# Kernel optimization log

Hardware: AMD Instinct MI355X
Metric: run time of the kernel (lower is better)

## Reference

```python
import jax, jax.numpy as jnp
import numpy as np

HEADS = 8


def setup_inputs() -> dict:
    key = jax.random.key(0)
    ks = jax.random.split(key, 4)
    b, n, dim, inner = 8, 1024, 512, 512
    x = jax.random.normal(ks[0], (b, n, dim), jnp.float32)
    cp_mask = jax.random.randint(ks[1], (n, n), 0, 2, jnp.int32)  # binary core-periphery mask
    w_qkv = jax.random.normal(ks[2], (dim, 3 * inner), jnp.float32) * 0.02
    w_out = jax.random.normal(ks[3], (inner, dim), jnp.float32) * 0.02
    b_out = jnp.zeros((dim,), jnp.float32)
    return {"x": x, "cp_mask": cp_mask, "w_qkv": w_qkv, "w_out": w_out,
            "b_out": b_out, "patches_in_core_nodes": 16}


def reference(x, cp_mask, w_qkv, w_out, b_out, patches_in_core_nodes):
    b, n, dim = x.shape
    inner = w_qkv.shape[1] // 3
    dh = inner // HEADS
    scale = dh ** -0.5

    qkv = x @ w_qkv                                   # [b, n, 3*inner]
    q, k, v = jnp.split(qkv, 3, axis=-1)
    split_heads = lambda t: t.reshape(b, n, HEADS, dh).transpose(0, 2, 1, 3)
    q, k, v = map(split_heads, (q, k, v))             # [b, h, n, dh]

    mask = cp_mask.astype(x.dtype)                    # [n, n]
    dots_raw = jnp.einsum('bhnd,bhmd->bhnm', q, k)    # [b, h, n, n]

    # analysis pass: per-row mean |masked score|, summed over heads (detached in original)
    nnz = jnp.count_nonzero(cp_mask, axis=1).astype(x.dtype)       # [n]
    score = (jnp.abs(dots_raw * mask) * scale).sum(axis=1).sum(axis=-1) / nnz  # [b, n]
    score = jax.lax.stop_gradient(score)
    # original: list(np.argsort(score)) then list.reverse() -> batch order reversed
    idx = jnp.argsort(score, axis=-1)[::-1]           # [b, n]

    attn = jax.nn.softmax(dots_raw * scale * mask, axis=-1)
    out = jnp.einsum('bhnm,bhmd->bhnd', attn, v)      # [b, h, n, dh]
    out = out.transpose(0, 2, 1, 3).reshape(b, n, inner)

    # sequential row swap: out[j,i] <-> out[j,idx[j,i]] using the pristine clone
    out_clone = out
    bi = jnp.arange(b)
    for i in range(1, patches_in_core_nodes + 1):
        ti = idx[:, i]                                # [b]
        out = out.at[bi, i].set(out_clone[bi, ti])
        out = out.at[bi, ti].set(out_clone[:, i])
    return out @ w_out + b_out
```

## Files before the change

kernel.cpp:

```cpp
#include <hip/hip_runtime.h>
#include <hip/hip_bf16.h>

#define NN 1024
#define DH 64
#define DIM 512
#define INNER 512
#define QKV_N 1536
#define SCALE 0.125f
#define KPITCH 72

typedef short short8 __attribute__((ext_vector_type(8)));
typedef float floatx4 __attribute__((ext_vector_type(4)));

static __device__ __forceinline__ unsigned short f2bf(float x) {
  __hip_bfloat16 h = __float2bfloat16(x);
  unsigned short u;
  __builtin_memcpy(&u, &h, 2);
  return u;
}
static __device__ __forceinline__ void splitbf(float x, unsigned short& hi, unsigned short& lo) {
  __hip_bfloat16 h = __float2bfloat16(x);
  float hf = __bfloat162float(h);
  __hip_bfloat16 l = __float2bfloat16(x - hf);
  __builtin_memcpy(&hi, &h, 2);
  __builtin_memcpy(&lo, &l, 2);
}
static __device__ __forceinline__ void gll16(const unsigned short* g, unsigned short* l) {
  __builtin_amdgcn_global_load_lds(
      (const __attribute__((address_space(1))) unsigned int*)g,
      (__attribute__((address_space(3))) unsigned int*)l, 16, 0, 0);
}

__global__ __launch_bounds__(64) void nnz_kernel(const int* __restrict__ mask,
                                                 float* __restrict__ nnzf,
                                                 unsigned long long* __restrict__ Mbits) {
  int row = blockIdx.x;
  int lane = threadIdx.x;
  const int* mrow = mask + (size_t)row * NN;
  int tot = 0;
  for (int mt = 0; mt < 16; ++mt) {
    unsigned long long bits = __ballot(mrow[mt * 64 + lane] != 0);
    if (lane == 0) {
      Mbits[(size_t)row * 16 + mt] = bits;
      tot += __popcll(bits);
    }
  }
  if (lane == 0) nnzf[row] = (float)tot;
}

__global__ __launch_bounds__(256) void split_kernel(const float* __restrict__ in,
                                                    unsigned short* __restrict__ hi,
                                                    unsigned short* __restrict__ lo,
                                                    int n4) {
  int i = blockIdx.x * 256 + threadIdx.x;
  if (i >= n4) return;
  float4 v = ((const float4*)in)[i];
  ushort4 h, l;
  splitbf(v.x, h.x, l.x);
  splitbf(v.y, h.y, l.y);
  splitbf(v.z, h.z, l.z);
  splitbf(v.w, h.w, l.w);
  ((ushort4*)hi)[i] = h;
  ((ushort4*)lo)[i] = l;
}

__global__ __launch_bounds__(256) void tsplit_kernel(const float* __restrict__ in, int K, int N,
                                                     unsigned short* __restrict__ hiT,
                                                     unsigned short* __restrict__ loT) {
  __shared__ float tile[32][33];
  int n0 = blockIdx.x * 32, k0 = blockIdx.y * 32;
  int t = threadIdx.x;
  int tn = t & 31, tk = t >> 5;
#pragma unroll
  for (int i = 0; i < 32; i += 8)
    tile[tk + i][tn] = in[(size_t)(k0 + tk + i) * N + n0 + tn];
  __syncthreads();
#pragma unroll
  for (int i = 0; i < 32; i += 8) {
    int n = tk + i;
    float v = tile[tn][n];
    unsigned short h, l;
    splitbf(v, h, l);
    hiT[(size_t)(n0 + n) * K + k0 + tn] = h;
    loT[(size_t)(n0 + n) * K + k0 + tn] = l;
  }
}

__global__ __launch_bounds__(256) void qkv_mfma(const unsigned short* __restrict__ xhi,
                                                const unsigned short* __restrict__ xlo,
                                                const unsigned short* __restrict__ bhiT,
                                                const unsigned short* __restrict__ bloT,
                                                unsigned short* __restrict__ qhi,
                                                unsigned short* __restrict__ qlo,
                                                unsigned short* __restrict__ khi,
                                                unsigned short* __restrict__ klo,
                                                unsigned short* __restrict__ vb) {
  __shared__ __align__(16) unsigned short Ah[128 * 32], Al[128 * 32];
  __shared__ __align__(16) unsigned short Bh[128 * 32], Bl[128 * 32];
  int t = threadIdx.x;
  int lane = t & 63, w = t >> 6;
  int wr = w >> 1, wc = w & 1;
  int s = lane & 15, q4 = lane >> 4;
  int r0 = blockIdx.y * 128, c0 = blockIdx.x * 128;
  int kcol = (lane & 3) * 8;
  int rA = lane >> 2;

  floatx4 acc[4][4];
#pragma unroll
  for (int mi = 0; mi < 4; ++mi)
#pragma unroll
    for (int ni = 0; ni < 4; ++ni) { acc[mi][ni][0] = 0.f; acc[mi][ni][1] = 0.f; acc[mi][ni][2] = 0.f; acc[mi][ni][3] = 0.f; }

  for (int kt = 0; kt < DIM; kt += 32) {
    __syncthreads();
#pragma unroll
    for (int c = 0; c < 2; ++c) {
      int chunk = w * 2 + c;
      int row = chunk * 16 + rA;
      int lo_off = chunk * 512;
      gll16(&xhi[(size_t)(r0 + row) * DIM + kt + kcol], &Ah[lo_off]);
      gll16(&xlo[(size_t)(r0 + row) * DIM + kt + kcol], &Al[lo_off]);
      gll16(&bhiT[(size_t)(c0 + row) * DIM + kt + kcol], &Bh[lo_off]);
      gll16(&bloT[(size_t)(c0 + row) * DIM + kt + kcol], &Bl[lo_off]);
    }
    __syncthreads();
    short8 ah[4], al[4], bhf[4], blf[4];
#pragma unroll
    for (int mi = 0; mi < 4; ++mi) {
      ah[mi] = *(const short8*)&Ah[(wr * 64 + mi * 16 + s) * 32 + q4 * 8];
      al[mi] = *(const short8*)&Al[(wr * 64 + mi * 16 + s) * 32 + q4 * 8];
    }
#pragma unroll
    for (int ni = 0; ni < 4; ++ni) {
      bhf[ni] = *(const short8*)&Bh[(wc * 64 + ni * 16 + s) * 32 + q4 * 8];
      blf[ni] = *(const short8*)&Bl[(wc * 64 + ni * 16 + s) * 32 + q4 * 8];
    }
#pragma unroll
    for (int mi = 0; mi < 4; ++mi)
#pragma unroll
      for (int ni = 0; ni < 4; ++ni) {
        acc[mi][ni] = __builtin_amdgcn_mfma_f32_16x16x32_bf16(al[mi], bhf[ni], acc[mi][ni], 0, 0, 0);
        acc[mi][ni] = __builtin_amdgcn_mfma_f32_16x16x32_bf16(ah[mi], blf[ni], acc[mi][ni], 0, 0, 0);
        acc[mi][ni] = __builtin_amdgcn_mfma_f32_16x16x32_bf16(ah[mi], bhf[ni], acc[mi][ni], 0, 0, 0);
      }
  }

  int which = c0 >> 9;
#pragma unroll
  for (int mi = 0; mi < 4; ++mi)
#pragma unroll
    for (int ni = 0; ni < 4; ++ni) {
      int Cl = c0 + wc * 64 + ni * 16 + s;
      int cc = Cl & 511, h = cc >> 6, d = cc & 63;
#pragma unroll
      for (int i = 0; i < 4; ++i) {
        int R = r0 + wr * 64 + mi * 16 + q4 * 4 + i;
        int b = R >> 10, n = R & 1023;
        size_t o = (size_t)((((b << 3) + h) << 10) + n) * DH + d;
        float v = acc[mi][ni][i];
        if (which == 0) {
          unsigned short hh, ll;
          splitbf(SCALE * v, hh, ll);
          qhi[o] = hh; qlo[o] = ll;
        } else if (which == 1) {
          unsigned short hh, ll;
          splitbf(v, hh, ll);
          khi[o] = hh; klo[o] = ll;
        } else {
          vb[o] = f2bf(v);
        }
      }
    }
}

__global__ __launch_bounds__(256) void vtrans(const unsigned short* __restrict__ vb,
                                              unsigned short* __restrict__ vT) {
  int bh = blockIdx.y, nt = blockIdx.x;
  __shared__ __align__(16) unsigned short T[64][KPITCH];
  int t = threadIdx.x;
  {
    int n = t >> 2, d0 = (t & 3) * 16;
    const unsigned short* src = &vb[((size_t)bh * NN + nt * 64 + n) * DH + d0];
    *(short8*)&T[n][d0] = *(const short8*)&src[0];
    *(short8*)&T[n][d0 + 8] = *(const short8*)&src[8];
  }
  __syncthreads();
  {
    int d = t >> 2, n0 = (t & 3) * 16;
    short8 o0, o1;
#pragma unroll
    for (int j = 0; j < 8; ++j) {
      o0[j] = (short)T[n0 + j][d];
      o1[j] = (short)T[n0 + 8 + j][d];
    }
    unsigned short* dst = &vT[((size_t)bh * DH + d) * NN + nt * 64 + n0];
    *(short8*)&dst[0] = o0;
    *(short8*)&dst[8] = o1;
  }
}

__global__ __launch_bounds__(256, 4) void attn_kernel(const unsigned short* __restrict__ qhi,
                                                      const unsigned short* __restrict__ qlo,
                                                      const unsigned short* __restrict__ khi,
                                                      const unsigned short* __restrict__ klo,
                                                      const unsigned short* __restrict__ vT,
                                                      const unsigned long long* __restrict__ Mbits,
                                                      unsigned short* __restrict__ ohi,
                                                      unsigned short* __restrict__ olo,
                                                      float* __restrict__ sph) {
  int l = blockIdx.y * 16 + blockIdx.x;
  int k = l >> 3;
  int rb = k & 15;
  int bh = (l & 7) + 8 * (k >> 4);
  int b = bh >> 3, h = bh & 7;
  int row0 = rb * 64;
  int t = threadIdx.x;
  int lane = t & 63, w = t >> 6;
  int q4 = lane >> 4, s = lane & 15;
  int gr = 16 * w + s;

  __shared__ __align__(16) unsigned short Khs[64][KPITCH], Kls[64][KPITCH];
  __shared__ __align__(16) unsigned short Vts[64][KPITCH];
  __shared__ __align__(16) unsigned short Pss[64][KPITCH];
  __shared__ unsigned long long Mb[64];

  short8 aqh[2], aql[2];
  {
    size_t qb0 = ((size_t)bh * NN + row0 + gr) * DH;
#pragma unroll
    for (int ks = 0; ks < 2; ++ks) {
      aqh[ks] = *(const short8*)&qhi[qb0 + ks * 32 + q4 * 8];
      aql[ks] = *(const short8*)&qlo[qb0 + ks * 32 + q4 * 8];
    }
  }

  floatx4 Oacc[4];
  float Lacc[4], Sco[4];
#pragma unroll
  for (int j = 0; j < 4; ++j) { Oacc[j][0] = 0.f; Oacc[j][1] = 0.f; Oacc[j][2] = 0.f; Oacc[j][3] = 0.f; }
#pragma unroll
  for (int i = 0; i < 4; ++i) { Lacc[i] = 0.f; Sco[i] = 0.f; }

  for (int mt = 0; mt < 16; ++mt) {
    int m0 = mt * 64;
    __syncthreads();
#pragma unroll
    for (int p = 0; p < 2; ++p) {
      int idx = p * 256 + t;
      int n = idx >> 3, c8 = (idx & 7) * 8;
      size_t g = ((size_t)bh * NN + m0 + n) * DH + c8;
      *(short8*)&Khs[n][c8] = *(const short8*)&khi[g];
      *(short8*)&Kls[n][c8] = *(const short8*)&klo[g];
      *(short8*)&Vts[n][c8] = *(const short8*)&vT[((size_t)bh * DH + n) * NN + m0 + c8];
    }
    if (t < 64) Mb[t] = Mbits[(size_t)(row0 + t) * 16 + mt];
    __syncthreads();

    floatx4 Sf[4];
#pragma unroll
    for (int j = 0; j < 4; ++j) { Sf[j][0] = 0.f; Sf[j][1] = 0.f; Sf[j][2] = 0.f; Sf[j][3] = 0.f; }
#pragma unroll
    for (int ks = 0; ks < 2; ++ks) {
      int d0 = ks * 32 + q4 * 8;
#pragma unroll
      for (int j = 0; j < 4; ++j) {
        short8 kh8 = *(const short8*)&Khs[16 * j + s][d0];
        short8 kl8 = *(const short8*)&Kls[16 * j + s][d0];
        Sf[j] = __builtin_amdgcn_mfma_f32_16x16x32_bf16(aql[ks], kh8, Sf[j], 0, 0, 0);
        Sf[j] = __builtin_amdgcn_mfma_f32_16x16x32_bf16(aqh[ks], kl8, Sf[j], 0, 0, 0);
        Sf[j] = __builtin_amdgcn_mfma_f32_16x16x32_bf16(aqh[ks], kh8, Sf[j], 0, 0, 0);
      }
    }

    unsigned long long mb[4];
#pragma unroll
    for (int i = 0; i < 4; ++i) mb[i] = Mb[16 * w + 4 * q4 + i];
    unsigned short pw[4][4];
#pragma unroll
    for (int j = 0; j < 4; ++j) {
#pragma unroll
      for (int i = 0; i < 4; ++i) {
        float sv = Sf[j][i];
        float mf = ((mb[i] >> (16 * j + s)) & 1ULL) ? 1.0f : 0.0f;
        Sco[i] += fabsf(sv) * mf;
        float p = __expf(sv * mf);
        Lacc[i] += p;
        pw[i][j] = f2bf(p);
      }
    }

#pragma unroll
    for (int i = 0; i < 4; ++i)
#pragma unroll
      for (int j = 0; j < 4; ++j) Pss[16 * w + 4 * q4 + i][16 * j + s] = pw[i][j];

#pragma unroll
    for (int ks = 0; ks < 2; ++ks) {
      int mm0 = ks * 32 + q4 * 8;
      short8 ap = *(const short8*)&Pss[gr][mm0];
#pragma unroll
      for (int j = 0; j < 4; ++j) {
        short8 bv = *(const short8*)&Vts[16 * j + s][mm0];
        Oacc[j] = __builtin_amdgcn_mfma_f32_16x16x32_bf16(ap, bv, Oacc[j], 0, 0, 0);
      }
    }
  }

#pragma unroll
  for (int off = 1; off < 16; off <<= 1) {
#pragma unroll
    for (int i = 0; i < 4; ++i) {
      Lacc[i] += __shfl_xor(Lacc[i], off, 16);
      Sco[i] += __shfl_xor(Sco[i], off, 16);
    }
  }
#pragma unroll
  for (int i = 0; i < 4; ++i) {
    int r = row0 + 16 * w + 4 * q4 + i;
    float iv = 1.0f / Lacc[i];
#pragma unroll
    for (int j = 0; j < 4; ++j) {
      float o = Oacc[j][i] * iv;
      unsigned short hh, ll;
      splitbf(o, hh, ll);
      size_t oo = (size_t)((b << 10) + r) * INNER + (h << 6) + 16 * j + s;
      ohi[oo] = hh; olo[oo] = ll;
    }
    if (s == 0) sph[((size_t)bh << 10) + r] = Sco[i];
  }
}

__global__ __launch_bounds__(256) void score_select(const float* __restrict__ sph,
                                                    const float* __restrict__ nnzf,
                                                    const int* __restrict__ pic_ptr,
                                                    int* __restrict__ asc) {
  int bb = blockIdx.x;
  int t = threadIdx.x;
  int cnt = pic_ptr[0] + 1;
  float v[4];
#pragma unroll
  for (int i = 0; i < 4; ++i) {
    int r = t + 256 * i;
    float sv = 0.f;
#pragma unroll
    for (int h = 0; h < 8; ++h) sv += sph[(size_t)(((bb << 3) + h) << 10) + r];
    v[i] = sv / nnzf[r];
  }
  __shared__ float wv[4];
  __shared__ int wi[4];
  __shared__ int bsel;
  for (int sel = 0; sel < cnt; ++sel) {
    float bv = v[0];
    int bi = t;
#pragma unroll
    for (int i = 1; i < 4; ++i) {
      if (v[i] < bv) { bv = v[i]; bi = t + 256 * i; }
    }
#pragma unroll
    for (int off = 1; off < 64; off <<= 1) {
      float ov = __shfl_xor(bv, off, 64);
      int oi = __shfl_xor(bi, off, 64);
      if (ov < bv || (ov == bv && oi < bi)) { bv = ov; bi = oi; }
    }
    if ((t & 63) == 0) { wv[t >> 6] = bv; wi[t >> 6] = bi; }
    __syncthreads();
    if (t == 0) {
      float B = wv[0]; int I = wi[0];
#pragma unroll
      for (int q = 1; q < 4; ++q) {
        if (wv[q] < B || (wv[q] == B && wi[q] < I)) { B = wv[q]; I = wi[q]; }
      }
      bsel = I;
      asc[bb * 32 + sel] = I;
    }
    __syncthreads();
    int wloc = bsel - t;
    if (wloc >= 0 && (wloc & 255) == 0 && wloc < 1024) v[wloc >> 8] = 3.4e38f;
    __syncthreads();
  }
}

__global__ __launch_bounds__(256) void build_src(const int* __restrict__ asc,
                                                 const int* __restrict__ pic_ptr,
                                                 int* __restrict__ src) {
  int bi = blockIdx.x;
  int t = threadIdx.x;
  for (int r = t; r < 1024; r += 256) src[bi * 1024 + r] = r;
  __syncthreads();
  if (t == 0) {
    int pic = pic_ptr[0];
    const int* a = &asc[(7 - bi) * 32];
    for (int i = 1; i <= pic; ++i) {
      int ti = a[i];
      src[bi * 1024 + i] = ti;
      src[bi * 1024 + ti] = i;
    }
  }
}

__global__ __launch_bounds__(256) void out_mfma(const unsigned short* __restrict__ ahi,
                                                const unsigned short* __restrict__ alo,
                                                const unsigned short* __restrict__ bhiT,
                                                const unsigned short* __restrict__ bloT,
                                                const float* __restrict__ bias,
                                                const int* __restrict__ src,
                                                float* __restrict__ C) {
  __shared__ __align__(16) unsigned short Ah[128 * 32], Al[128 * 32];
  __shared__ __align__(16) unsigned short Bh[128 * 32], Bl[128 * 32];
  int t = threadIdx.x;
  int lane = t & 63, w = t >> 6;
  int wr = w >> 1, wc = w & 1;
  int s = lane & 15, q4 = lane >> 4;
  int r0 = blockIdx.y * 128, c0 = blockIdx.x * 128;
  int bb = r0 >> 10;
  int kcol = (lane & 3) * 8;
  int rA = lane >> 2;

  int grow[2];
#pragma unroll
  for (int c = 0; c < 2; ++c) {
    int row = (w * 2 + c) * 16 + rA;
    grow[c] = (bb << 10) + src[r0 + row];
  }

  floatx4 acc[4][4];
#pragma unroll
  for (int mi = 0; mi < 4; ++mi)
#pragma unroll
    for (int ni = 0; ni < 4; ++ni) { acc[mi][ni][0] = 0.f; acc[mi][ni][1] = 0.f; acc[mi][ni][2] = 0.f; acc[mi][ni][3] = 0.f; }

  for (int kt = 0; kt < INNER; kt += 32) {
    __syncthreads();
#pragma unroll
    for (int c = 0; c < 2; ++c) {
      int chunk = w * 2 + c;
      int row = chunk * 16 + rA;
      int lo_off = chunk * 512;
      gll16(&ahi[(size_t)grow[c] * INNER + kt + kcol], &Ah[lo_off]);
      gll16(&alo[(size_t)grow[c] * INNER + kt + kcol], &Al[lo_off]);
      gll16(&bhiT[(size_t)(c0 + row) * INNER + kt + kcol], &Bh[lo_off]);
      gll16(&bloT[(size_t)(c0 + row) * INNER + kt + kcol], &Bl[lo_off]);
    }
    __syncthreads();
    short8 ah[4], al[4], bhf[4], blf[4];
#pragma unroll
    for (int mi = 0; mi < 4; ++mi) {
      ah[mi] = *(const short8*)&Ah[(wr * 64 + mi * 16 + s) * 32 + q4 * 8];
      al[mi] = *(const short8*)&Al[(wr * 64 + mi * 16 + s) * 32 + q4 * 8];
    }
#pragma unroll
    for (int ni = 0; ni < 4; ++ni) {
      bhf[ni] = *(const short8*)&Bh[(wc * 64 + ni * 16 + s) * 32 + q4 * 8];
      blf[ni] = *(const short8*)&Bl[(wc * 64 + ni * 16 + s) * 32 + q4 * 8];
    }
#pragma unroll
    for (int mi = 0; mi < 4; ++mi)
#pragma unroll
      for (int ni = 0; ni < 4; ++ni) {
        acc[mi][ni] = __builtin_amdgcn_mfma_f32_16x16x32_bf16(al[mi], bhf[ni], acc[mi][ni], 0, 0, 0);
        acc[mi][ni] = __builtin_amdgcn_mfma_f32_16x16x32_bf16(ah[mi], blf[ni], acc[mi][ni], 0, 0, 0);
        acc[mi][ni] = __builtin_amdgcn_mfma_f32_16x16x32_bf16(ah[mi], bhf[ni], acc[mi][ni], 0, 0, 0);
      }
  }

#pragma unroll
  for (int ni = 0; ni < 4; ++ni) {
    int Cl = c0 + wc * 64 + ni * 16 + s;
    float bv = bias[Cl];
#pragma unroll
    for (int mi = 0; mi < 4; ++mi)
#pragma unroll
      for (int i = 0; i < 4; ++i) {
        int R = r0 + wr * 64 + mi * 16 + q4 * 4 + i;
        C[(size_t)R * DIM + Cl] = acc[mi][ni][i] + bv;
      }
  }
}

extern "C" void kernel_launch(void* const* d_in, const int* in_sizes, int n_in,
                              void* d_out, int out_size, void* d_ws, size_t ws_size,
                              hipStream_t stream) {
  const float* x      = (const float*)d_in[0];
  const int*   cpmask = (const int*)d_in[1];
  const float* w_qkv  = (const float*)d_in[2];
  const float* w_out  = (const float*)d_in[3];
  const float* b_out  = (const float*)d_in[4];
  const int*   pic    = (const int*)d_in[5];
  float* out = (float*)d_out;

  unsigned short* xhi   = (unsigned short*)d_ws;
  unsigned short* xlo   = xhi + 4194304;
  unsigned short* wqhiT = xlo + 4194304;
  unsigned short* wqloT = wqhiT + 786432;
  unsigned short* wohiT = wqloT + 786432;
  unsigned short* woloT = wohiT + 262144;
  unsigned short* qhi   = woloT + 262144;
  unsigned short* qlo   = qhi + 4194304;
  unsigned short* khi   = qlo + 4194304;
  unsigned short* klo   = khi + 4194304;
  unsigned short* vbp   = klo + 4194304;
  float* sph  = (float*)(vbp + 4194304);
  float* sc   = sph + 65536;
  float* nnzf = sc + 8192;
  int*   asc  = (int*)(nnzf + 1024);
  int*   src  = asc + 512;
  unsigned long long* Mbits = (unsigned long long*)(src + 8192);
  unsigned short* vTp = (unsigned short*)(Mbits + 16384);

  unsigned short* ohi = xhi;
  unsigned short* olo = xlo;

  hipLaunchKernelGGL(nnz_kernel,    dim3(1024),    dim3(64),  0, stream, cpmask, nnzf, Mbits);
  hipLaunchKernelGGL(split_kernel,  dim3(4096),    dim3(256), 0, stream, x, xhi, xlo, 1048576);
  hipLaunchKernelGGL(tsplit_kernel, dim3(48, 16),  dim3(256), 0, stream, w_qkv, DIM, QKV_N, wqhiT, wqloT);
  hipLaunchKernelGGL(tsplit_kernel, dim3(16, 16),  dim3(256), 0, stream, w_out, INNER, DIM, wohiT, woloT);
  hipLaunchKernelGGL(qkv_mfma,      dim3(12, 64),  dim3(256), 0, stream, xhi, xlo, wqhiT, wqloT,
                     qhi, qlo, khi, klo, vbp);
  hipLaunchKernelGGL(vtrans,        dim3(16, 64),  dim3(256), 0, stream, vbp, vTp);
  hipLaunchKernelGGL(attn_kernel,   dim3(16, 64),  dim3(256), 0, stream, qhi, qlo, khi, klo, vTp,
                     Mbits, ohi, olo, sph);
  hipLaunchKernelGGL(score_select,  dim3(8),       dim3(256), 0, stream, sph, nnzf, pic, asc);
  hipLaunchKernelGGL(build_src,     dim3(8),       dim3(256), 0, stream, asc, pic, src);
  hipLaunchKernelGGL(out_mfma,      dim3(4, 64),   dim3(256), 0, stream, ohi, olo, wohiT, woloT,
                     b_out, src, out);
}
```

Baseline: 258.6 us.

## Restage GEMMs with swizzled 64-wide K tiles, fuse V transpose, vectorize stores

The QKV and output GEMMs now stage 64-wide K tiles with XOR-swizzled LDS layouts, one operand plane per wave, and a 1D grid ordered by row tile. The V projection uses a single bf16 pass instead of three split passes and writes V transposed straight from an LDS staging tile, which removes the separate vtrans kernel. The attention kernel loads K, K-lo and V^T through async global-to-LDS copies into swizzled tiles, reads a mask-bits array transposed for coalescing, and writes its output through LDS as vectorized short8 stores. Together these target LDS bank conflicts, scattered 2-byte global stores and launch overhead, at the cost of a much larger QKV shared-memory footprint (about 66 KB) and lower occupancy.

```diff
diff --git a/kernel.cpp b/kernel.cpp
--- a/kernel.cpp
+++ b/kernel.cpp
@@ -7,7 +7,7 @@
 #define INNER 512
 #define QKV_N 1536
 #define SCALE 0.125f
-#define KPITCH 72
+#define PPITCH 72
 
 typedef short short8 __attribute__((ext_vector_type(8)));
 typedef float floatx4 __attribute__((ext_vector_type(4)));
@@ -41,7 +41,7 @@
   for (int mt = 0; mt < 16; ++mt) {
     unsigned long long bits = __ballot(mrow[mt * 64 + lane] != 0);
     if (lane == 0) {
-      Mbits[(size_t)row * 16 + mt] = bits;
+      Mbits[(size_t)mt * NN + row] = bits;
       tot += __popcll(bits);
     }
   }
@@ -94,16 +94,38 @@
                                                 unsigned short* __restrict__ qlo,
                                                 unsigned short* __restrict__ khi,
                                                 unsigned short* __restrict__ klo,
-                                                unsigned short* __restrict__ vb) {
-  __shared__ __align__(16) unsigned short Ah[128 * 32], Al[128 * 32];
-  __shared__ __align__(16) unsigned short Bh[128 * 32], Bl[128 * 32];
+                                                unsigned short* __restrict__ vT) {
+  __shared__ __align__(16) unsigned char smemQ[67584];
+  unsigned short* planeS = (unsigned short*)smemQ;
+  float* ct = (float*)smemQ;
+
+  int l = blockIdx.x;
+  int by = l & 63, bx = l >> 6;
+  int r0 = by * 128, c0 = bx * 128;
+  int which = c0 >> 9;
+  bool split3 = (which != 2);
   int t = threadIdx.x;
   int lane = t & 63, w = t >> 6;
   int wr = w >> 1, wc = w & 1;
   int s = lane & 15, q4 = lane >> 4;
-  int r0 = blockIdx.y * 128, c0 = blockIdx.x * 128;
-  int kcol = (lane & 3) * 8;
-  int rA = lane >> 2;
+  int sx7 = s & 7;
+  int r8 = lane >> 3, j7 = lane & 7;
+  int colsw = ((j7 ^ r8) << 3);
+
+  const unsigned short* gsrc;
+  int tb;
+  if (w == 0) { gsrc = xhi; tb = r0; }
+  else if (w == 1) { gsrc = xlo; tb = r0; }
+  else if (w == 2) { gsrc = bhiT; tb = c0; }
+  else { gsrc = bloT; tb = c0; }
+  unsigned short* lp = planeS + w * 8192;
+  const unsigned short* gp = gsrc + (size_t)(tb + r8) * DIM + colsw;
+  bool doStage = split3 || (w == 0) || (w == 2);
+
+  const unsigned short* Ah = planeS;
+  const unsigned short* Al = planeS + 8192;
+  const unsigned short* Bh = planeS + 16384;
+  const unsigned short* Bl = planeS + 24576;
 
   floatx4 acc[4][4];
 #pragma unroll
@@ -111,91 +133,106 @@
 #pragma unroll
     for (int ni = 0; ni < 4; ++ni) { acc[mi][ni][0] = 0.f; acc[mi][ni][1] = 0.f; acc[mi][ni][2] = 0.f; acc[mi][ni][3] = 0.f; }
 
-  for (int kt = 0; kt < DIM; kt += 32) {
-    __syncthreads();
-#pragma unroll
-    for (int c = 0; c < 2; ++c) {
-      int chunk = w * 2 + c;
-      int row = chunk * 16 + rA;
-      int lo_off = chunk * 512;
-      gll16(&xhi[(size_t)(r0 + row) * DIM + kt + kcol], &Ah[lo_off]);
-      gll16(&xlo[(size_t)(r0 + row) * DIM + kt + kcol], &Al[lo_off]);
-      gll16(&bhiT[(size_t)(c0 + row) * DIM + kt + kcol], &Bh[lo_off]);
-      gll16(&bloT[(size_t)(c0 + row) * DIM + kt + kcol], &Bl[lo_off]);
-    }
-    __syncthreads();
-    short8 ah[4], al[4], bhf[4], blf[4];
-#pragma unroll
-    for (int mi = 0; mi < 4; ++mi) {
-      ah[mi] = *(const short8*)&Ah[(wr * 64 + mi * 16 + s) * 32 + q4 * 8];
-      al[mi] = *(const short8*)&Al[(wr * 64 + mi * 16 + s) * 32 + q4 * 8];
-    }
-#pragma unroll
-    for (int ni = 0; ni < 4; ++ni) {
-      bhf[ni] = *(const short8*)&Bh[(wc * 64 + ni * 16 + s) * 32 + q4 * 8];
-      blf[ni] = *(const short8*)&Bl[(wc * 64 + ni * 16 + s) * 32 + q4 * 8];
-    }
+  for (int kt = 0; kt < DIM; kt += 64) {
+    __syncthreads();
+    if (doStage) {
+#pragma unroll
+      for (int ii = 0; ii < 16; ++ii)
+        gll16(gp + (size_t)ii * 8 * DIM + kt, lp + ii * 512);
+    }
+    __syncthreads();
+#pragma unroll
+    for (int ks2 = 0; ks2 < 2; ++ks2) {
+      int pc = ((ks2 * 4 + q4) ^ sx7) << 3;
+      short8 ah[4], al[4], bhf[4], blf[4];
+#pragma unroll
+      for (int mi = 0; mi < 4; ++mi) {
+        int ra = (wr * 64 + mi * 16 + s) * 64 + pc;
+        ah[mi] = *(const short8*)&Ah[ra];
+        if (split3) al[mi] = *(const short8*)&Al[ra];
+      }
+#pragma unroll
+      for (int ni = 0; ni < 4; ++ni) {
+        int rb = (wc * 64 + ni * 16 + s) * 64 + pc;
+        bhf[ni] = *(const short8*)&Bh[rb];
+        if (split3) blf[ni] = *(const short8*)&Bl[rb];
+      }
+#pragma unroll
+      for (int mi = 0; mi < 4; ++mi)
+#pragma unroll
+        for (int ni = 0; ni < 4; ++ni) {
+          if (split3) {
+            acc[mi][ni] = __builtin_amdgcn_mfma_f32_16x16x32_bf16(al[mi], bhf[ni], acc[mi][ni], 0, 0, 0);
+            acc[mi][ni] = __builtin_amdgcn_mfma_f32_16x16x32_bf16(ah[mi], blf[ni], acc[mi][ni], 0, 0, 0);
+          }
+          acc[mi][ni] = __builtin_amdgcn_mfma_f32_16x16x32_bf16(ah[mi], bhf[ni], acc[mi][ni], 0, 0, 0);
+        }
+    }
+  }
+
+  __syncthreads();
+  if (which != 2) {
+    float sc = (which == 0) ? SCALE : 1.0f;
 #pragma unroll
     for (int mi = 0; mi < 4; ++mi)
 #pragma unroll
-      for (int ni = 0; ni < 4; ++ni) {
-        acc[mi][ni] = __builtin_amdgcn_mfma_f32_16x16x32_bf16(al[mi], bhf[ni], acc[mi][ni], 0, 0, 0);
-        acc[mi][ni] = __builtin_amdgcn_mfma_f32_16x16x32_bf16(ah[mi], blf[ni], acc[mi][ni], 0, 0, 0);
-        acc[mi][ni] = __builtin_amdgcn_mfma_f32_16x16x32_bf16(ah[mi], bhf[ni], acc[mi][ni], 0, 0, 0);
-      }
-  }
-
-  int which = c0 >> 9;
-#pragma unroll
-  for (int mi = 0; mi < 4; ++mi)
-#pragma unroll
-    for (int ni = 0; ni < 4; ++ni) {
-      int Cl = c0 + wc * 64 + ni * 16 + s;
-      int cc = Cl & 511, h = cc >> 6, d = cc & 63;
-#pragma unroll
-      for (int i = 0; i < 4; ++i) {
-        int R = r0 + wr * 64 + mi * 16 + q4 * 4 + i;
-        int b = R >> 10, n = R & 1023;
-        size_t o = (size_t)((((b << 3) + h) << 10) + n) * DH + d;
-        float v = acc[mi][ni][i];
-        if (which == 0) {
-          unsigned short hh, ll;
-          splitbf(SCALE * v, hh, ll);
-          qhi[o] = hh; qlo[o] = ll;
-        } else if (which == 1) {
-          unsigned short hh, ll;
-          splitbf(v, hh, ll);
-          khi[o] = hh; klo[o] = ll;
-        } else {
-          vb[o] = f2bf(v);
-        }
-      }
-    }
-}
-
-__global__ __launch_bounds__(256) void vtrans(const unsigned short* __restrict__ vb,
-                                              unsigned short* __restrict__ vT) {
-  int bh = blockIdx.y, nt = blockIdx.x;
-  __shared__ __align__(16) unsigned short T[64][KPITCH];
-  int t = threadIdx.x;
-  {
-    int n = t >> 2, d0 = (t & 3) * 16;
-    const unsigned short* src = &vb[((size_t)bh * NN + nt * 64 + n) * DH + d0];
-    *(short8*)&T[n][d0] = *(const short8*)&src[0];
-    *(short8*)&T[n][d0 + 8] = *(const short8*)&src[8];
+      for (int ni = 0; ni < 4; ++ni)
+#pragma unroll
+        for (int i = 0; i < 4; ++i)
+          ct[(wr * 64 + mi * 16 + q4 * 4 + i) * 132 + (wc * 64 + ni * 16 + s)] = acc[mi][ni][i] * sc;
+  } else {
+#pragma unroll
+    for (int mi = 0; mi < 4; ++mi)
+#pragma unroll
+      for (int ni = 0; ni < 4; ++ni)
+#pragma unroll
+        for (int i = 0; i < 4; ++i)
+          ct[(wc * 64 + ni * 16 + s) * 132 + (wr * 64 + mi * 16 + q4 * 4 + i)] = acc[mi][ni][i];
   }
   __syncthreads();
-  {
-    int d = t >> 2, n0 = (t & 3) * 16;
-    short8 o0, o1;
-#pragma unroll
-    for (int j = 0; j < 8; ++j) {
-      o0[j] = (short)T[n0 + j][d];
-      o1[j] = (short)T[n0 + 8 + j][d];
-    }
-    unsigned short* dst = &vT[((size_t)bh * DH + d) * NN + nt * 64 + n0];
-    *(short8*)&dst[0] = o0;
-    *(short8*)&dst[8] = o1;
+  if (which != 2) {
+    int tr = t >> 1, ch = t & 1;
+    int R = r0 + tr, b = R >> 10, n = R & 1023;
+    int h0 = ((c0 & 511) >> 6) + ch;
+    unsigned short* dhi = (which == 0) ? qhi : khi;
+    unsigned short* dlo = (which == 0) ? qlo : klo;
+    size_t go = ((size_t)(((b << 3) + h0) << 10) + n) * DH;
+#pragma unroll
+    for (int u = 0; u < 4; ++u) {
+      const float* src = &ct[tr * 132 + ch * 64 + u * 16];
+      short8 h8a, h8b, l8a, l8b;
+#pragma unroll
+      for (int e = 0; e < 8; ++e) {
+        unsigned short hh, ll;
+        splitbf(src[e], hh, ll);
+        h8a[e] = (short)hh; l8a[e] = (short)ll;
+        splitbf(src[8 + e], hh, ll);
+        h8b[e] = (short)hh; l8b[e] = (short)ll;
+      }
+      *(short8*)&dhi[go + u * 16] = h8a;
+      *(short8*)&dhi[go + u * 16 + 8] = h8b;
+      *(short8*)&dlo[go + u * 16] = l8a;
+      *(short8*)&dlo[go + u * 16 + 8] = l8b;
+    }
+  } else {
+    int cr = t >> 1, th = t & 1;
+    int b = r0 >> 10;
+    int hglob = ((c0 & 511) >> 6) + (cr >> 6);
+    int d = cr & 63;
+    int n0 = (r0 & 1023) + th * 64;
+    size_t go = ((size_t)(((b << 3) + hglob) * DH) + d) * NN + n0;
+#pragma unroll
+    for (int u = 0; u < 4; ++u) {
+      const float* src = &ct[cr * 132 + th * 64 + u * 16];
+      short8 o0, o1;
+#pragma unroll
+      for (int e = 0; e < 8; ++e) {
+        o0[e] = (short)f2bf(src[e]);
+        o1[e] = (short)f2bf(src[8 + e]);
+      }
+      *(short8*)&vT[go + u * 16] = o0;
+      *(short8*)&vT[go + u * 16 + 8] = o1;
+    }
   }
 }
 
@@ -204,7 +241,7 @@
                                                       const unsigned short* __restrict__ khi,
                                                       const unsigned short* __restrict__ klo,
                                                       const unsigned short* __restrict__ vT,
-                                                      const unsigned long long* __restrict__ Mbits,
+                                                      const unsigned long long* __restrict__ MbT,
                                                       unsigned short* __restrict__ ohi,
                                                       unsigned short* __restrict__ olo,
                                                       float* __restrict__ sph) {
@@ -217,12 +254,22 @@
   int t = threadIdx.x;
   int lane = t & 63, w = t >> 6;
   int q4 = lane >> 4, s = lane & 15;
+  int sx7 = s & 7;
   int gr = 16 * w + s;
-
-  __shared__ __align__(16) unsigned short Khs[64][KPITCH], Kls[64][KPITCH];
-  __shared__ __align__(16) unsigned short Vts[64][KPITCH];
-  __shared__ __align__(16) unsigned short Pss[64][KPITCH];
+  int r8 = lane >> 3, j7 = lane & 7;
+  int colsw = ((j7 ^ r8) << 3);
+
+  __shared__ __align__(16) unsigned short stageS[3 * 4096];
+  __shared__ __align__(16) unsigned short Ps[64 * PPITCH];
   __shared__ unsigned long long Mb[64];
+  unsigned short* Khs = stageS;
+  unsigned short* Kls = stageS + 4096;
+  unsigned short* Vts = stageS + 8192;
+  float* Ofl = (float*)stageS;
+
+  const unsigned short* khp = khi + ((size_t)bh * NN + 16 * w + r8) * DH + colsw;
+  const unsigned short* klp = klo + ((size_t)bh * NN + 16 * w + r8) * DH + colsw;
+  const unsigned short* vtp = vT + ((size_t)bh * DH + 16 * w + r8) * NN + colsw;
 
   short8 aqh[2], aql[2];
   {
@@ -242,18 +289,15 @@
   for (int i = 0; i < 4; ++i) { Lacc[i] = 0.f; Sco[i] = 0.f; }
 
   for (int mt = 0; mt < 16; ++mt) {
-    int m0 = mt * 64;
-    __syncthreads();
-#pragma unroll
-    for (int p = 0; p < 2; ++p) {
-      int idx = p * 256 + t;
-      int n = idx >> 3, c8 = (idx & 7) * 8;
-      size_t g = ((size_t)bh * NN + m0 + n) * DH + c8;
-      *(short8*)&Khs[n][c8] = *(const short8*)&khi[g];
-      *(short8*)&Kls[n][c8] = *(const short8*)&klo[g];
-      *(short8*)&Vts[n][c8] = *(const short8*)&vT[((size_t)bh * DH + n) * NN + m0 + c8];
-    }
-    if (t < 64) Mb[t] = Mbits[(size_t)(row0 + t) * 16 + mt];
+    __syncthreads();
+#pragma unroll
+    for (int ii = 0; ii < 2; ++ii) {
+      int lofs = (16 * w + 8 * ii) * 64;
+      gll16(khp + (size_t)mt * 64 * DH + (size_t)ii * 8 * DH, Khs + lofs);
+      gll16(klp + (size_t)mt * 64 * DH + (size_t)ii * 8 * DH, Kls + lofs);
+      gll16(vtp + (size_t)mt * 64 + (size_t)ii * 8 * NN, Vts + lofs);
+    }
+    if (t < 64) Mb[t] = MbT[(size_t)mt * NN + row0 + t];
     __syncthreads();
 
     floatx4 Sf[4];
@@ -261,11 +305,12 @@
     for (int j = 0; j < 4; ++j) { Sf[j][0] = 0.f; Sf[j][1] = 0.f; Sf[j][2] = 0.f; Sf[j][3] = 0.f; }
 #pragma unroll
     for (int ks = 0; ks < 2; ++ks) {
-      int d0 = ks * 32 + q4 * 8;
+      int pc = ((ks * 4 + q4) ^ sx7) << 3;
 #pragma unroll
       for (int j = 0; j < 4; ++j) {
-        short8 kh8 = *(const short8*)&Khs[16 * j + s][d0];
-        short8 kl8 = *(const short8*)&Kls[16 * j + s][d0];
+        int rk = (16 * j + s) * 64 + pc;
+        short8 kh8 = *(const short8*)&Khs[rk];
+        short8 kl8 = *(const short8*)&Kls[rk];
         Sf[j] = __builtin_amdgcn_mfma_f32_16x16x32_bf16(aql[ks], kh8, Sf[j], 0, 0, 0);
         Sf[j] = __builtin_amdgcn_mfma_f32_16x16x32_bf16(aqh[ks], kl8, Sf[j], 0, 0, 0);
         Sf[j] = __builtin_amdgcn_mfma_f32_16x16x32_bf16(aqh[ks], kh8, Sf[j], 0, 0, 0);
@@ -292,15 +337,16 @@
 #pragma unroll
     for (int i = 0; i < 4; ++i)
 #pragma unroll
-      for (int j = 0; j < 4; ++j) Pss[16 * w + 4 * q4 + i][16 * j + s] = pw[i][j];
+      for (int j = 0; j < 4; ++j) Ps[(16 * w + 4 * q4 + i) * PPITCH + 16 * j + s] = pw[i][j];
 
 #pragma unroll
     for (int ks = 0; ks < 2; ++ks) {
       int mm0 = ks * 32 + q4 * 8;
-      short8 ap = *(const short8*)&Pss[gr][mm0];
+      short8 ap = *(const short8*)&Ps[gr * PPITCH + mm0];
+      int pc = ((ks * 4 + q4) ^ sx7) << 3;
 #pragma unroll
       for (int j = 0; j < 4; ++j) {
-        short8 bv = *(const short8*)&Vts[16 * j + s][mm0];
+        short8 bv = *(const short8*)&Vts[(16 * j + s) * 64 + pc];
         Oacc[j] = __builtin_amdgcn_mfma_f32_16x16x32_bf16(ap, bv, Oacc[j], 0, 0, 0);
       }
     }
@@ -314,19 +360,39 @@
       Sco[i] += __shfl_xor(Sco[i], off, 16);
     }
   }
+  if (s == 0) {
+#pragma unroll
+    for (int i = 0; i < 4; ++i)
+      sph[((size_t)bh << 10) + row0 + 16 * w + 4 * q4 + i] = Sco[i];
+  }
+
+  __syncthreads();
 #pragma unroll
   for (int i = 0; i < 4; ++i) {
-    int r = row0 + 16 * w + 4 * q4 + i;
     float iv = 1.0f / Lacc[i];
 #pragma unroll
-    for (int j = 0; j < 4; ++j) {
-      float o = Oacc[j][i] * iv;
+    for (int j = 0; j < 4; ++j)
+      Ofl[(16 * w + 4 * q4 + i) * 68 + 16 * j + s] = Oacc[j][i] * iv;
+  }
+  __syncthreads();
+  {
+    int tr = t >> 2, dq = t & 3;
+    int r = row0 + tr;
+    size_t go = ((size_t)((b << 10) + r)) * INNER + (h << 6) + dq * 16;
+    const float* src = &Ofl[tr * 68 + dq * 16];
+    short8 h8a, h8b, l8a, l8b;
+#pragma unroll
+    for (int e = 0; e < 8; ++e) {
       unsigned short hh, ll;
-      splitbf(o, hh, ll);
-      size_t oo = (size_t)((b << 10) + r) * INNER + (h << 6) + 16 * j + s;
-      ohi[oo] = hh; olo[oo] = ll;
-    }
-    if (s == 0) sph[((size_t)bh << 10) + r] = Sco[i];
+      splitbf(src[e], hh, ll);
+      h8a[e] = (short)hh; l8a[e] = (short)ll;
+      splitbf(src[8 + e], hh, ll);
+      h8b[e] = (short)hh; l8b[e] = (short)ll;
+    }
+    *(short8*)&ohi[go] = h8a;
+    *(short8*)&ohi[go + 8] = h8b;
+    *(short8*)&olo[go] = l8a;
+    *(short8*)&olo[go + 8] = l8b;
   }
 }
 
@@ -405,23 +471,31 @@
                                                 const float* __restrict__ bias,
                                                 const int* __restrict__ src,
                                                 float* __restrict__ C) {
-  __shared__ __align__(16) unsigned short Ah[128 * 32], Al[128 * 32];
-  __shared__ __align__(16) unsigned short Bh[128 * 32], Bl[128 * 32];
+  __shared__ __align__(16) unsigned short planeS[4 * 8192];
+  int l = blockIdx.x;
+  int by = l & 63, bx = l >> 6;
+  int r0 = by * 128, c0 = bx * 128;
   int t = threadIdx.x;
   int lane = t & 63, w = t >> 6;
   int wr = w >> 1, wc = w & 1;
   int s = lane & 15, q4 = lane >> 4;
-  int r0 = blockIdx.y * 128, c0 = blockIdx.x * 128;
-  int bb = r0 >> 10;
-  int kcol = (lane & 3) * 8;
-  int rA = lane >> 2;
-
-  int grow[2];
-#pragma unroll
-  for (int c = 0; c < 2; ++c) {
-    int row = (w * 2 + c) * 16 + rA;
-    grow[c] = (bb << 10) + src[r0 + row];
-  }
+  int sx7 = s & 7;
+  int r8 = lane >> 3, j7 = lane & 7;
+  int colsw = ((j7 ^ r8) << 3);
+  int bb1024 = (r0 >> 10) << 10;
+
+  int srcrow[16];
+  if (w < 2) {
+#pragma unroll
+    for (int ii = 0; ii < 16; ++ii) srcrow[ii] = src[r0 + ii * 8 + r8];
+  }
+  const unsigned short* gsrc = (w == 0) ? ahi : (w == 1) ? alo : (w == 2) ? bhiT : bloT;
+  unsigned short* lp = planeS + w * 8192;
+
+  const unsigned short* Ah = planeS;
+  const unsigned short* Al = planeS + 8192;
+  const unsigned short* Bh = planeS + 16384;
+  const unsigned short* Bl = planeS + 24576;
 
   floatx4 acc[4][4];
 #pragma unroll
@@ -429,38 +503,43 @@
 #pragma unroll
     for (int ni = 0; ni < 4; ++ni) { acc[mi][ni][0] = 0.f; acc[mi][ni][1] = 0.f; acc[mi][ni][2] = 0.f; acc[mi][ni][3] = 0.f; }
 
-  for (int kt = 0; kt < INNER; kt += 32) {
-    __syncthreads();
-#pragma unroll
-    for (int c = 0; c < 2; ++c) {
-      int chunk = w * 2 + c;
-      int row = chunk * 16 + rA;
-      int lo_off = chunk * 512;
-      gll16(&ahi[(size_t)grow[c] * INNER + kt + kcol], &Ah[lo_off]);
-      gll16(&alo[(size_t)grow[c] * INNER + kt + kcol], &Al[lo_off]);
-      gll16(&bhiT[(size_t)(c0 + row) * INNER + kt + kcol], &Bh[lo_off]);
-      gll16(&bloT[(size_t)(c0 + row) * INNER + kt + kcol], &Bl[lo_off]);
-    }
-    __syncthreads();
-    short8 ah[4], al[4], bhf[4], blf[4];
-#pragma unroll
-    for (int mi = 0; mi < 4; ++mi) {
-      ah[mi] = *(const short8*)&Ah[(wr * 64 + mi * 16 + s) * 32 + q4 * 8];
-      al[mi] = *(const short8*)&Al[(wr * 64 + mi * 16 + s) * 32 + q4 * 8];
-    }
-#pragma unroll
-    for (int ni = 0; ni < 4; ++ni) {
-      bhf[ni] = *(const short8*)&Bh[(wc * 64 + ni * 16 + s) * 32 + q4 * 8];
-      blf[ni] = *(const short8*)&Bl[(wc * 64 + ni * 16 + s) * 32 + q4 * 8];
-    }
-#pragma unroll
-    for (int mi = 0; mi < 4; ++mi)
+  for (int kt = 0; kt < INNER; kt += 64) {
+    __syncthreads();
+    if (w < 2) {
+#pragma unroll
+      for (int ii = 0; ii < 16; ++ii)
+        gll16(gsrc + (size_t)(bb1024 + srcrow[ii]) * INNER + kt + colsw, lp + ii * 512);
+    } else {
+#pragma unroll
+      for (int ii = 0; ii < 16; ++ii)
+        gll16(gsrc + (size_t)(c0 + ii * 8 + r8) * INNER + kt + colsw, lp + ii * 512);
+    }
+    __syncthreads();
+#pragma unroll
+    for (int ks2 = 0; ks2 < 2; ++ks2) {
+      int pc = ((ks2 * 4 + q4) ^ sx7) << 3;
+      short8 ah[4], al[4], bhf[4], blf[4];
+#pragma unroll
+      for (int mi = 0; mi < 4; ++mi) {
+        int ra = (wr * 64 + mi * 16 + s) * 64 + pc;
+        ah[mi] = *(const short8*)&Ah[ra];
+        al[mi] = *(const short8*)&Al[ra];
+      }
 #pragma unroll
       for (int ni = 0; ni < 4; ++ni) {
-        acc[mi][ni] = __builtin_amdgcn_mfma_f32_16x16x32_bf16(al[mi], bhf[ni], acc[mi][ni], 0, 0, 0);
-        acc[mi][ni] = __builtin_amdgcn_mfma_f32_16x16x32_bf16(ah[mi], blf[ni], acc[mi][ni], 0, 0, 0);
-        acc[mi][ni] = __builtin_amdgcn_mfma_f32_16x16x32_bf16(ah[mi], bhf[ni], acc[mi][ni], 0, 0, 0);
-      }
+        int rb = (wc * 64 + ni * 16 + s) * 64 + pc;
+        bhf[ni] = *(const short8*)&Bh[rb];
+        blf[ni] = *(const short8*)&Bl[rb];
+      }
+#pragma unroll
+      for (int mi = 0; mi < 4; ++mi)
+#pragma unroll
+        for (int ni = 0; ni < 4; ++ni) {
+          acc[mi][ni] = __builtin_amdgcn_mfma_f32_16x16x32_bf16(al[mi], bhf[ni], acc[mi][ni], 0, 0, 0);
+          acc[mi][ni] = __builtin_amdgcn_mfma_f32_16x16x32_bf16(ah[mi], blf[ni], acc[mi][ni], 0, 0, 0);
+          acc[mi][ni] = __builtin_amdgcn_mfma_f32_16x16x32_bf16(ah[mi], bhf[ni], acc[mi][ni], 0, 0, 0);
+        }
+    }
   }
 
 #pragma unroll
@@ -514,13 +593,12 @@
   hipLaunchKernelGGL(split_kernel,  dim3(4096),    dim3(256), 0, stream, x, xhi, xlo, 1048576);
   hipLaunchKernelGGL(tsplit_kernel, dim3(48, 16),  dim3(256), 0, stream, w_qkv, DIM, QKV_N, wqhiT, wqloT);
   hipLaunchKernelGGL(tsplit_kernel, dim3(16, 16),  dim3(256), 0, stream, w_out, INNER, DIM, wohiT, woloT);
-  hipLaunchKernelGGL(qkv_mfma,      dim3(12, 64),  dim3(256), 0, stream, xhi, xlo, wqhiT, wqloT,
-                     qhi, qlo, khi, klo, vbp);
-  hipLaunchKernelGGL(vtrans,        dim3(16, 64),  dim3(256), 0, stream, vbp, vTp);
+  hipLaunchKernelGGL(qkv_mfma,      dim3(768),     dim3(256), 0, stream, xhi, xlo, wqhiT, wqloT,
+                     qhi, qlo, khi, klo, vTp);
   hipLaunchKernelGGL(attn_kernel,   dim3(16, 64),  dim3(256), 0, stream, qhi, qlo, khi, klo, vTp,
                      Mbits, ohi, olo, sph);
   hipLaunchKernelGGL(score_select,  dim3(8),       dim3(256), 0, stream, sph, nnzf, pic, asc);
   hipLaunchKernelGGL(build_src,     dim3(8),       dim3(256), 0, stream, asc, pic, src);
-  hipLaunchKernelGGL(out_mfma,      dim3(4, 64),   dim3(256), 0, stream, ohi, olo, wohiT, woloT,
+  hipLaunchKernelGGL(out_mfma,      dim3(256),     dim3(256), 0, stream, ohi, olo, wohiT, woloT,
                      b_out, src, out);
 }
```

Result: faster. 226.5 us (-12.4%).
